# Optimization experiments

Hardware: AMD Instinct MI355X
Metric: run time of the kernel (lower is better)

## Reference

```python
import jax, jax.numpy as jnp
import numpy as np

B, C, L, D, P = 64, 64, 720, 512, 336
P2, H = P // 2, 512  # H = hidden width of the ProbG branch


def setup_inputs() -> dict:
    key = jax.random.key(0)
    ks = jax.random.split(key, 20)
    def w(k, i, o):
        return jax.random.normal(k, (i, o), jnp.float32) / np.sqrt(i)
    return {
        "x_bsd": jax.random.normal(ks[0], (B, L, C), jnp.float32),
        "z0": jax.random.normal(ks[1], (B, C, D), jnp.float32),
        "y0": jax.random.normal(ks[2], (B, C, P), jnp.float32),
        # ProbG hidden branch (HID_GIVEN_X_V0 -> SS_Z_GIVEN_X_V0)
        "W_h": w(ks[3], L, H),
        "W_ssz": w(ks[4], H, 2 * D),
        # x->z scale/shift flows (versions v2..v5)
        "W_xz_v2": w(ks[5], L, 2 * D),
        "W_xz_v3": w(ks[6], L, 2 * D),
        "W_xz_v4": w(ks[7], L, 2 * D),
        "W_xz_v5": w(ks[8], L, 2 * D),
        # z->x scale/shift flows (v0, v2, v3, v5)
        "W_zx_v0": w(ks[9], D, 2 * L),
        "W_zx_v2": w(ks[10], D, 2 * L),
        "W_zx_v3": w(ks[11], D, 2 * L),
        "W_zx_v5": w(ks[12], D, 2 * L),
        # z->y scale/shift flow (v4, used inside encoding)
        "W_zy_v4": w(ks[13], D, 2 * P),
        # decode heads: ROT_IN_Y_V1 and KOO_Y_GIVEN_Z_V0
        "W_rot": w(ks[14], D, P2),
        "W_koo": w(ks[15], D, 2 * P),
        # Koopman complex params for y-space (a + i b per channel/pair)
        "a_y": jnp.ones((C, P2), jnp.float32),
        "b_y": jnp.zeros((C, P2), jnp.float32) + 0.1,
    }


def _ss(params):
    """Split conditioner output into (positive scale, shift)."""
    s_raw, t = jnp.split(params, 2, axis=-1)
    return jnp.exp(jnp.tanh(s_raw)), t


def _affine(v, cond, W):
    """Scale/shift flow: v <- v * s(cond) + t(cond)."""
    s, t = _ss(jnp.einsum('bck,km->bcm', cond, W))
    return v * s + t


def _rot(u, theta, inv=False):
    """Rotate interleaved (re, im) pairs of u [B,C,P] by angles theta [B,C,P/2]."""
    re, im = u[..., 0::2], u[..., 1::2]
    th = -theta if inv else theta
    c, s = jnp.cos(th), jnp.sin(th)
    return jnp.stack([c * re - s * im, s * re + c * im], axis=-1).reshape(u.shape)


def _koop(u, a, b, inv=False):
    """Koopman unit-complex multiply on interleaved pairs; a,b [C,P/2]."""
    n = jnp.sqrt(a * a + b * b)
    ca, cb = a / n, b / n
    cb = -cb if inv else cb
    re, im = u[..., 0::2], u[..., 1::2]
    return jnp.stack([ca * re - cb * im, cb * re + ca * im], axis=-1).reshape(u.shape)


def reference(x_bsd, z0, y0, W_h, W_ssz, W_xz_v2, W_xz_v3, W_xz_v4, W_xz_v5,
              W_zx_v0, W_zx_v2, W_zx_v3, W_zx_v5, W_zy_v4, W_rot, W_koo, a_y, b_y):
    x = jnp.transpose(x_bsd, (0, 2, 1))  # [B,C,L]
    z = z0 * 0.1                          # [B,C,D]
    y = y0 * 0.1                          # [B,C,P]
    # ---- encoding phase ----
    h = jax.nn.gelu(jnp.einsum('bcl,lk->bck', x, W_h))  # X_to_Z_PROB hidden
    z = _affine(z, h, W_ssz)
    x = _affine(x, z, W_zx_v0)
    z = _affine(z, x, W_xz_v2); x = _affine(x, z, W_zx_v2)
    z = _affine(z, x, W_xz_v3); x = _affine(x, z, W_zx_v3)
    z = _affine(z, x, W_xz_v4); y = _affine(y, z, W_zy_v4)  # Z_to_Y_V4
    z = _affine(z, x, W_xz_v5); x = _affine(x, z, W_zx_v5)
    pre_y = y
    # ---- decode: rotate -> ky -> scale -> ky.inv -> rot.inv -> shift ----
    theta = jnp.pi * jnp.tanh(jnp.einsum('bcd,dp->bcp', z, W_rot))   # [B,C,P/2]
    scale, shift = _ss(jnp.einsum('bcd,dp->bcp', z, W_koo))          # [B,C,P]
    const = _koop(_rot(pre_y, theta), a_y, b_y)
    accu = const * scale
    accu = _rot(_koop(accu, a_y, b_y, inv=True), theta, inv=True) + shift
    return jnp.transpose(accu, (0, 2, 1))  # [B,P,C]
```

## Files before the change

kernel.cpp:

```cpp
#include <hip/hip_runtime.h>
#include <hip/hip_bf16.h>
#include <math.h>

#define BB  64
#define CC  64
#define LL  720
#define LLP 736
#define DD  512
#define PP  336
#define P2C 168
#define HH  512
#define MM  (BB*CC)

typedef _Float16 f16x8 __attribute__((ext_vector_type(8)));
typedef float    f32x4 __attribute__((ext_vector_type(4)));

#define GLDS16(g, l) __builtin_amdgcn_global_load_lds( \
    (const __attribute__((address_space(1))) void*)(g), \
    (__attribute__((address_space(3))) void*)(l), 16, 0, 0)

struct WDesc { const float* src; _Float16* dstHi; _Float16* dstLo;
               int K, N, Kpad, tbase, tilesN; };
struct WTab  { WDesc d[12]; };

__global__ __launch_bounds__(256) void k_convert(WTab tab) {
  __shared__ float tile[16][17];
  const int bid = blockIdx.x;
  int wi = 0;
#pragma unroll
  for (int i = 1; i < 12; ++i) if (bid >= tab.d[i].tbase) wi = i;
  const WDesc d = tab.d[wi];
  const int lt = bid - d.tbase;
  const int tk = lt / d.tilesN, tn = lt % d.tilesN;
  const int k0 = tk * 16, n0 = tn * 16;
  const int tx = threadIdx.x & 15, ty = threadIdx.x >> 4;
  float v = 0.f;
  if (n0 + tx < d.N) v = d.src[(size_t)(k0 + ty) * d.N + n0 + tx];
  tile[ty][tx] = v;
  __syncthreads();
  if (n0 + ty < d.N) {
    const float w = tile[tx][ty];
    const _Float16 h = (_Float16)w;
    const _Float16 l = (_Float16)(w - (float)h);
    const size_t base = (size_t)(n0 + ty) * d.Kpad;
    d.dstHi[base + k0 + tx] = h;
    d.dstLo[base + k0 + tx] = l;
    if (d.Kpad != d.K && k0 + 16 == d.K) {
      d.dstHi[base + d.K + tx] = (_Float16)0.f;
      d.dstLo[base + d.K + tx] = (_Float16)0.f;
    }
  }
}

__global__ __launch_bounds__(256) void k_xpose(const float* __restrict__ xbsd,
                                               _Float16* __restrict__ xhi,
                                               _Float16* __restrict__ xlo) {
  __shared__ float tile[16][17];
  const int b = blockIdx.z, l0 = blockIdx.x * 16, c0 = blockIdx.y * 16;
  const int tx = threadIdx.x, ty = threadIdx.y;
  tile[ty][tx] = xbsd[(size_t)b * LL * CC + (size_t)(l0 + ty) * CC + c0 + tx];
  __syncthreads();
  const float v = tile[tx][ty];
  const _Float16 h = (_Float16)v;
  const _Float16 l = (_Float16)(v - (float)h);
  const size_t m = (size_t)b * CC + c0 + ty;
  xhi[m * LLP + l0 + tx] = h;
  xlo[m * LLP + l0 + tx] = l;
  if (l0 == 704) {
    xhi[m * LLP + 720 + tx] = (_Float16)0.f;
    xlo[m * LLP + 720 + tx] = (_Float16)0.f;
  }
}

template<int EPI, bool DUAL, bool VIN16, bool OUT_T>
__global__ __launch_bounds__(256)
void k_gemm(const _Float16* Ahi, const _Float16* Alo, int lda,
            const _Float16* Whi, const _Float16* Wlo, int ldw,
            const float* Vin32, const _Float16* VinHi,
            const _Float16* VinLo, int ldv, float vscale,
            float* outT32,
            _Float16* outHi, _Float16* outLo, int ldo,
            int Kp, int Nv) {
  constexpr int NB   = DUAL ? 128 : 64;
  constexpr int BBUF = NB * 32;
  constexpr int SBUF = 2 * BBUF;
  constexpr int NCH  = 2 * (NB / 16);
  constexpr int NCHW = NCH / 4;
  __shared__ _Float16 smem[2 * SBUF];

  const int m0 = blockIdx.y * 64;
  const int n0 = blockIdx.x * 64;
  const int tid = threadIdx.x;
  const int w = tid >> 6, lane = tid & 63, q = lane >> 4, r = lane & 15;
  const int wr = (w & 1) * 32, wc = (w >> 1) * 32;
  const int lr = lane >> 2, ls = lane & 3;

  f32x4 accS[2][2] = {};
  f32x4 accT[2][2] = {};

  auto stage = [&](int kc, int bsel) {
    const int k0 = kc << 5;
    _Float16* sb = smem + bsel * SBUF;
#pragma unroll
    for (int cc = 0; cc < NCHW; ++cc) {
      const int chunk = w * NCHW + cc;
      const _Float16* gsrc;
      _Float16* ldst;
      if (chunk < NB / 16) {
        const int rb = chunk * 16;
        const int R = rb + lr;
        const int ss = ls ^ ((R >> 1) & 3);
        const int wrow = (R < 64) ? (n0 + R) : (Nv + n0 + (R - 64));
        gsrc = Whi + (size_t)wrow * ldw + k0 + ss * 8;
        ldst = sb + rb * 32;
      } else {
        const int rb = (chunk - NB / 16) * 16;
        const int R = rb + lr;
        const int ss = ls ^ ((R >> 1) & 3);
        const int wrow = (R < 64) ? (n0 + R) : (Nv + n0 + (R - 64));
        gsrc = Wlo + (size_t)wrow * ldw + k0 + ss * 8;
        ldst = sb + BBUF + rb * 32;
      }
      GLDS16(gsrc, ldst);
    }
  };

  const _Float16* aH0 = Ahi + (size_t)(m0 + wr + r)      * lda + q * 8;
  const _Float16* aH1 = Ahi + (size_t)(m0 + wr + 16 + r) * lda + q * 8;
  const _Float16* aL0 = Alo + (size_t)(m0 + wr + r)      * lda + q * 8;
  const _Float16* aL1 = Alo + (size_t)(m0 + wr + 16 + r) * lda + q * 8;

  const int nk = Kp >> 5;
  stage(0, 0);
  f16x8 c0h = *(const f16x8*)(aH0);
  f16x8 c1h = *(const f16x8*)(aH1);
  f16x8 c0l = *(const f16x8*)(aL0);
  f16x8 c1l = *(const f16x8*)(aL1);
  f16x8 p0h = c0h, p1h = c1h, p0l = c0l, p1l = c1l;
  int cur = 0;
  for (int kc = 0; kc < nk; ++kc) {
    __syncthreads();
    if (kc + 1 < nk) {
      stage(kc + 1, cur ^ 1);
      const int ko = (kc + 1) << 5;
      p0h = *(const f16x8*)(aH0 + ko);
      p1h = *(const f16x8*)(aH1 + ko);
      p0l = *(const f16x8*)(aL0 + ko);
      p1l = *(const f16x8*)(aL1 + ko);
    }
    const _Float16* sb = smem + cur * SBUF;

#pragma unroll
    for (int ct = 0; ct < 2; ++ct) {
      const int RB = wc + ct * 16 + r;
      const int tb = (q ^ ((RB >> 1) & 3)) * 8;
      const f16x8 bh = *(const f16x8*)(sb + RB * 32 + tb);
      const f16x8 bl = *(const f16x8*)(sb + BBUF + RB * 32 + tb);
      accS[0][ct] = __builtin_amdgcn_mfma_f32_16x16x32_f16(c0h, bh, accS[0][ct], 0, 0, 0);
      accS[0][ct] = __builtin_amdgcn_mfma_f32_16x16x32_f16(c0l, bh, accS[0][ct], 0, 0, 0);
      accS[0][ct] = __builtin_amdgcn_mfma_f32_16x16x32_f16(c0h, bl, accS[0][ct], 0, 0, 0);
      accS[1][ct] = __builtin_amdgcn_mfma_f32_16x16x32_f16(c1h, bh, accS[1][ct], 0, 0, 0);
      accS[1][ct] = __builtin_amdgcn_mfma_f32_16x16x32_f16(c1l, bh, accS[1][ct], 0, 0, 0);
      accS[1][ct] = __builtin_amdgcn_mfma_f32_16x16x32_f16(c1h, bl, accS[1][ct], 0, 0, 0);
      if (DUAL) {
        const int RT = 64 + RB;
        const int tt = (q ^ ((RT >> 1) & 3)) * 8;
        const f16x8 chh = *(const f16x8*)(sb + RT * 32 + tt);
        const f16x8 cll = *(const f16x8*)(sb + BBUF + RT * 32 + tt);
        accT[0][ct] = __builtin_amdgcn_mfma_f32_16x16x32_f16(c0h, chh, accT[0][ct], 0, 0, 0);
        accT[0][ct] = __builtin_amdgcn_mfma_f32_16x16x32_f16(c0l, chh, accT[0][ct], 0, 0, 0);
        accT[0][ct] = __builtin_amdgcn_mfma_f32_16x16x32_f16(c0h, cll, accT[0][ct], 0, 0, 0);
        accT[1][ct] = __builtin_amdgcn_mfma_f32_16x16x32_f16(c1h, chh, accT[1][ct], 0, 0, 0);
        accT[1][ct] = __builtin_amdgcn_mfma_f32_16x16x32_f16(c1l, chh, accT[1][ct], 0, 0, 0);
        accT[1][ct] = __builtin_amdgcn_mfma_f32_16x16x32_f16(c1h, cll, accT[1][ct], 0, 0, 0);
      }
    }
    c0h = p0h; c1h = p1h; c0l = p0l; c1l = p1l;
    cur ^= 1;
  }

#pragma unroll
  for (int rt = 0; rt < 2; ++rt) {
    const int mb = m0 + wr + rt * 16 + q * 4;
#pragma unroll
    for (int ct = 0; ct < 2; ++ct) {
      const int n = n0 + wc + ct * 16 + r;
      if (n >= Nv) continue;
      if (EPI == 2) {
        *(f32x4*)(outT32 + (size_t)n * MM + mb) = accS[rt][ct];
      } else if (EPI == 1) {
#pragma unroll
        for (int g = 0; g < 4; ++g) {
          const int m = mb + g;
          const float v = accS[rt][ct][g];
          const float o = 0.5f * v * (1.0f + tanhf(0.7978845608028654f * (v + 0.044715f * v * v * v)));
          const _Float16 h = (_Float16)o;
          outHi[(size_t)m * ldo + n] = h;
          outLo[(size_t)m * ldo + n] = (_Float16)(o - (float)h);
        }
      } else {
        f32x4 o;
#pragma unroll
        for (int g = 0; g < 4; ++g) {
          const int m = mb + g;
          float v;
          if (VIN16) {
            v = (float)VinHi[(size_t)m * ldv + n] + (float)VinLo[(size_t)m * ldv + n];
          } else {
            v = Vin32[(size_t)m * ldv + n];
          }
          const float s = expf(tanhf(accS[rt][ct][g]));
          o[g] = v * vscale * s + accT[rt][ct][g];
        }
        if (OUT_T) {
          *(f32x4*)(outT32 + (size_t)n * MM + mb) = o;
        } else {
#pragma unroll
          for (int g = 0; g < 4; ++g) {
            const int m = mb + g;
            const _Float16 h = (_Float16)o[g];
            outHi[(size_t)m * ldo + n] = h;
            outLo[(size_t)m * ldo + n] = (_Float16)(o[g] - (float)h);
          }
        }
      }
    }
  }
}

__global__ __launch_bounds__(256) void k_final(const float* __restrict__ Pt,
                                               const float* __restrict__ yT,
                                               const float* __restrict__ Ay,
                                               const float* __restrict__ By,
                                               float* __restrict__ out) {
  const int c = threadIdx.x;
  const int j = blockIdx.x * 4 + threadIdx.y;
  const int b = blockIdx.y;
  const int m = b * 64 + c;
  const float th = 3.14159265358979323846f * tanhf(Pt[(size_t)j * MM + m]);
  const float sc0 = expf(tanhf(Pt[(size_t)(168 + 2 * j) * MM + m]));
  const float sc1 = expf(tanhf(Pt[(size_t)(169 + 2 * j) * MM + m]));
  const float t0 = Pt[(size_t)(504 + 2 * j) * MM + m];
  const float t1 = Pt[(size_t)(505 + 2 * j) * MM + m];
  const float re = yT[(size_t)(2 * j) * MM + m];
  const float im = yT[(size_t)(2 * j + 1) * MM + m];
  const float a = Ay[c * P2C + j], bb = By[c * P2C + j];
  const float rn = rsqrtf(a * a + bb * bb);
  const float ca = a * rn, cb = bb * rn;
  float s1v, c1;
  sincosf(th, &s1v, &c1);
  const float r1 = c1 * re - s1v * im, i1 = s1v * re + c1 * im;
  const float r2 = ca * r1 - cb * i1,  i2 = cb * r1 + ca * i1;
  const float r3 = r2 * sc0,           i3 = i2 * sc1;
  const float r4 = ca * r3 + cb * i3,  i4 = ca * i3 - cb * r3;
  const float r5 = c1 * r4 + s1v * i4, i5 = c1 * i4 - s1v * r4;
  out[(size_t)b * PP * CC + (size_t)(2 * j) * CC + c]     = r5 + t0;
  out[(size_t)b * PP * CC + (size_t)(2 * j + 1) * CC + c] = i5 + t1;
}

extern "C" void kernel_launch(void* const* d_in, const int* in_sizes, int n_in,
                              void* d_out, int out_size, void* d_ws, size_t ws_size,
                              hipStream_t stream) {
  const float* x_bsd   = (const float*)d_in[0];
  const float* z0      = (const float*)d_in[1];
  const float* y0      = (const float*)d_in[2];
  const float* W_h     = (const float*)d_in[3];
  const float* W_ssz   = (const float*)d_in[4];
  const float* W_xz_v2 = (const float*)d_in[5];
  const float* W_xz_v3 = (const float*)d_in[6];
  const float* W_xz_v4 = (const float*)d_in[7];
  const float* W_xz_v5 = (const float*)d_in[8];
  const float* W_zx_v0 = (const float*)d_in[9];
  const float* W_zx_v2 = (const float*)d_in[10];
  const float* W_zx_v3 = (const float*)d_in[11];
  const float* W_zy_v4 = (const float*)d_in[13];
  const float* W_rot   = (const float*)d_in[14];
  const float* W_koo   = (const float*)d_in[15];
  const float* a_y     = (const float*)d_in[16];
  const float* b_y     = (const float*)d_in[17];
  float* out = (float*)d_out;

  char* p = (char*)d_ws;
  auto alloc = [&](size_t bytes) -> void* {
    void* r = (void*)p; p += (bytes + 255) & ~(size_t)255; return r;
  };
  float*    yT  = (float*)alloc((size_t)PP * MM * 4);
  float*    Pt  = (float*)alloc((size_t)(P2C * 5) * MM * 4);
  _Float16* xhi = (_Float16*)alloc((size_t)MM * LLP * 2);
  _Float16* xlo = (_Float16*)alloc((size_t)MM * LLP * 2);
  _Float16* zhi = (_Float16*)alloc((size_t)MM * DD * 2);
  _Float16* zlo = (_Float16*)alloc((size_t)MM * DD * 2);
  _Float16* hhi = (_Float16*)alloc((size_t)MM * HH * 2);
  _Float16* hlo = (_Float16*)alloc((size_t)MM * HH * 2);
  auto wpair = [&](size_t elems, _Float16** lo) -> _Float16* {
    _Float16* hi = (_Float16*)alloc(elems * 2);
    *lo = (_Float16*)alloc(elems * 2);
    return hi;
  };
  _Float16 *tWhL, *tWsszL, *tWxz2L, *tWxz3L, *tWxz4L, *tWxz5L;
  _Float16 *tWzx0L, *tWzx2L, *tWzx3L, *tWzyL, *tWcatL;
  _Float16* tWh   = wpair((size_t)HH * LLP, &tWhL);
  _Float16* tWssz = wpair((size_t)(2*DD) * DD, &tWsszL);
  _Float16* tWxz2 = wpair((size_t)(2*DD) * LLP, &tWxz2L);
  _Float16* tWxz3 = wpair((size_t)(2*DD) * LLP, &tWxz3L);
  _Float16* tWxz4 = wpair((size_t)(2*DD) * LLP, &tWxz4L);
  _Float16* tWxz5 = wpair((size_t)(2*DD) * LLP, &tWxz5L);
  _Float16* tWzx0 = wpair((size_t)1536 * DD, &tWzx0L);
  _Float16* tWzx2 = wpair((size_t)1536 * DD, &tWzx2L);
  _Float16* tWzx3 = wpair((size_t)1536 * DD, &tWzx3L);
  _Float16* tWzy  = wpair((size_t)768 * DD, &tWzyL);
  _Float16* tWcat = wpair((size_t)896 * DD, &tWcatL);

  WTab tab;
  int base = 0;
  auto put = [&](int i, const float* src, _Float16* dh, _Float16* dl,
                 int K, int N, int Kpad) {
    const int tN = (N + 15) / 16;
    tab.d[i] = WDesc{src, dh, dl, K, N, Kpad, base, tN};
    base += ((K + 15) / 16) * tN;
  };
  put(0,  W_h,     tWh,   tWhL,   LL, HH,   LLP);
  put(1,  W_ssz,   tWssz, tWsszL, DD, 2*DD, DD);
  put(2,  W_xz_v2, tWxz2, tWxz2L, LL, 2*DD, LLP);
  put(3,  W_xz_v3, tWxz3, tWxz3L, LL, 2*DD, LLP);
  put(4,  W_xz_v4, tWxz4, tWxz4L, LL, 2*DD, LLP);
  put(5,  W_xz_v5, tWxz5, tWxz5L, LL, 2*DD, LLP);
  put(6,  W_zx_v0, tWzx0, tWzx0L, DD, 2*LL, DD);
  put(7,  W_zx_v2, tWzx2, tWzx2L, DD, 2*LL, DD);
  put(8,  W_zx_v3, tWzx3, tWzx3L, DD, 2*LL, DD);
  put(9,  W_zy_v4, tWzy,  tWzyL,  DD, 2*PP, DD);
  put(10, W_rot,   tWcat, tWcatL, DD, P2C,  DD);
  put(11, W_koo,   tWcat + (size_t)P2C * DD, tWcatL + (size_t)P2C * DD, DD, 2*PP, DD);
  const int total_tiles = base;

  k_convert<<<dim3(total_tiles), dim3(256), 0, stream>>>(tab);
  k_xpose<<<dim3(45, 4, 64), dim3(16, 16), 0, stream>>>(x_bsd, xhi, xlo);

  const dim3 blk(256);
  k_gemm<1, false, false, false><<<dim3(8, 64), blk, 0, stream>>>(
      xhi, xlo, LLP, tWh, tWhL, LLP,
      nullptr, nullptr, nullptr, 0, 0.f, nullptr, hhi, hlo, HH, LLP, HH);
  k_gemm<0, true, false, false><<<dim3(8, 64), blk, 0, stream>>>(
      hhi, hlo, HH, tWssz, tWsszL, DD,
      z0, nullptr, nullptr, DD, 0.1f, nullptr, zhi, zlo, DD, DD, DD);
  k_gemm<0, true, true, false><<<dim3(12, 64), blk, 0, stream>>>(
      zhi, zlo, DD, tWzx0, tWzx0L, DD,
      nullptr, xhi, xlo, LLP, 1.f, nullptr, xhi, xlo, LLP, DD, LL);
  k_gemm<0, true, true, false><<<dim3(8, 64), blk, 0, stream>>>(
      xhi, xlo, LLP, tWxz2, tWxz2L, LLP,
      nullptr, zhi, zlo, DD, 1.f, nullptr, zhi, zlo, DD, LLP, DD);
  k_gemm<0, true, true, false><<<dim3(12, 64), blk, 0, stream>>>(
      zhi, zlo, DD, tWzx2, tWzx2L, DD,
      nullptr, xhi, xlo, LLP, 1.f, nullptr, xhi, xlo, LLP, DD, LL);
  k_gemm<0, true, true, false><<<dim3(8, 64), blk, 0, stream>>>(
      xhi, xlo, LLP, tWxz3, tWxz3L, LLP,
      nullptr, zhi, zlo, DD, 1.f, nullptr, zhi, zlo, DD, LLP, DD);
  k_gemm<0, true, true, false><<<dim3(12, 64), blk, 0, stream>>>(
      zhi, zlo, DD, tWzx3, tWzx3L, DD,
      nullptr, xhi, xlo, LLP, 1.f, nullptr, xhi, xlo, LLP, DD, LL);
  k_gemm<0, true, true, false><<<dim3(8, 64), blk, 0, stream>>>(
      xhi, xlo, LLP, tWxz4, tWxz4L, LLP,
      nullptr, zhi, zlo, DD, 1.f, nullptr, zhi, zlo, DD, LLP, DD);
  k_gemm<0, true, false, true><<<dim3(6, 64), blk, 0, stream>>>(
      zhi, zlo, DD, tWzy, tWzyL, DD,
      y0, nullptr, nullptr, PP, 0.1f, yT, nullptr, nullptr, 0, DD, PP);
  k_gemm<0, true, true, false><<<dim3(8, 64), blk, 0, stream>>>(
      xhi, xlo, LLP, tWxz5, tWxz5L, LLP,
      nullptr, zhi, zlo, DD, 1.f, nullptr, zhi, zlo, DD, LLP, DD);
  k_gemm<2, false, false, true><<<dim3(14, 64), blk, 0, stream>>>(
      zhi, zlo, DD, tWcat, tWcatL, DD,
      nullptr, nullptr, nullptr, 0, 0.f, Pt, nullptr, nullptr, 0, DD, P2C * 5);
  k_final<<<dim3(42, 64), dim3(64, 4), 0, stream>>>(Pt, yT, a_y, b_y, out);
}
```

Measured before the change: 514.9 us.

## Give each wave private B staging, swizzle block order, use fast transcendentals

After: 542.0 us. +5.3%, slower.

```diff
diff --git a/kernel.cpp b/kernel.cpp
--- a/kernel.cpp
+++ b/kernel.cpp
@@ -18,6 +18,13 @@
 #define GLDS16(g, l) __builtin_amdgcn_global_load_lds( \
     (const __attribute__((address_space(1))) void*)(g), \
     (__attribute__((address_space(3))) void*)(l), 16, 0, 0)
+
+__device__ __forceinline__ float ftanh(float x) {
+  const float ax = fabsf(x);
+  const float e  = __expf(2.f * ax);
+  const float t  = 1.f - 2.f / (e + 1.f);
+  return copysignf(t, x);
+}
 
 struct WDesc { const float* src; _Float16* dstHi; _Float16* dstLo;
                int K, N, Kpad, tbase, tilesN; };
@@ -81,47 +88,40 @@
             float* outT32,
             _Float16* outHi, _Float16* outLo, int ldo,
             int Kp, int Nv) {
-  constexpr int NB   = DUAL ? 128 : 64;
-  constexpr int BBUF = NB * 32;
-  constexpr int SBUF = 2 * BBUF;
-  constexpr int NCH  = 2 * (NB / 16);
-  constexpr int NCHW = NCH / 4;
-  __shared__ _Float16 smem[2 * SBUF];
-
-  const int m0 = blockIdx.y * 64;
-  const int n0 = blockIdx.x * 64;
+  constexpr int NBW  = DUAL ? 64 : 32;
+  constexpr int WBUF = NBW * 32;
+  constexpr int NCH  = 2 * (NBW / 16);
+  __shared__ _Float16 smem[4 * 2 * WBUF];
+
+  const int gx  = gridDim.x;
+  const int nwg = gx * gridDim.y;
+  const int id  = blockIdx.y * gx + blockIdx.x;
+  const int nid = (id & 7) * (nwg >> 3) + (id >> 3);
+  const int m0 = (nid / gx) * 64;
+  const int n0 = (nid % gx) * 64;
+
   const int tid = threadIdx.x;
   const int w = tid >> 6, lane = tid & 63, q = lane >> 4, r = lane & 15;
   const int wr = (w & 1) * 32, wc = (w >> 1) * 32;
   const int lr = lane >> 2, ls = lane & 3;
 
+  _Float16* wbase = smem + w * (2 * WBUF);
+
   f32x4 accS[2][2] = {};
   f32x4 accT[2][2] = {};
 
-  auto stage = [&](int kc, int bsel) {
+  auto stageB = [&](int kc) {
     const int k0 = kc << 5;
-    _Float16* sb = smem + bsel * SBUF;
-#pragma unroll
-    for (int cc = 0; cc < NCHW; ++cc) {
-      const int chunk = w * NCHW + cc;
-      const _Float16* gsrc;
-      _Float16* ldst;
-      if (chunk < NB / 16) {
-        const int rb = chunk * 16;
-        const int R = rb + lr;
-        const int ss = ls ^ ((R >> 1) & 3);
-        const int wrow = (R < 64) ? (n0 + R) : (Nv + n0 + (R - 64));
-        gsrc = Whi + (size_t)wrow * ldw + k0 + ss * 8;
-        ldst = sb + rb * 32;
-      } else {
-        const int rb = (chunk - NB / 16) * 16;
-        const int R = rb + lr;
-        const int ss = ls ^ ((R >> 1) & 3);
-        const int wrow = (R < 64) ? (n0 + R) : (Nv + n0 + (R - 64));
-        gsrc = Wlo + (size_t)wrow * ldw + k0 + ss * 8;
-        ldst = sb + BBUF + rb * 32;
-      }
-      GLDS16(gsrc, ldst);
+#pragma unroll
+    for (int cc = 0; cc < NCH; ++cc) {
+      const int pl   = (cc >= NCH / 2) ? 1 : 0;
+      const int rb   = (cc % (NCH / 2)) * 16;
+      const int lrow = rb + lr;
+      const int ss   = ls ^ ((lrow >> 1) & 3);
+      const int wrow = (lrow < 32) ? (n0 + wc + lrow)
+                                   : (Nv + n0 + wc + (lrow - 32));
+      const _Float16* g = (pl ? Wlo : Whi) + (size_t)wrow * ldw + k0 + ss * 8;
+      GLDS16(g, wbase + pl * WBUF + rb * 32);
     }
   };
 
@@ -131,52 +131,60 @@
   const _Float16* aL1 = Alo + (size_t)(m0 + wr + 16 + r) * lda + q * 8;
 
   const int nk = Kp >> 5;
-  stage(0, 0);
+  stageB(0);
   f16x8 c0h = *(const f16x8*)(aH0);
   f16x8 c1h = *(const f16x8*)(aH1);
   f16x8 c0l = *(const f16x8*)(aL0);
   f16x8 c1l = *(const f16x8*)(aL1);
   f16x8 p0h = c0h, p1h = c1h, p0l = c0l, p1l = c1l;
-  int cur = 0;
+
   for (int kc = 0; kc < nk; ++kc) {
-    __syncthreads();
+    asm volatile("s_waitcnt vmcnt(0)" ::: "memory");
+    __builtin_amdgcn_sched_barrier(0);
+
+    f16x8 bhS[2], blS[2], bhT[2], blT[2];
+#pragma unroll
+    for (int ct = 0; ct < 2; ++ct) {
+      const int rs = ct * 16 + r;
+      const int tb = (q ^ ((rs >> 1) & 3)) * 8;
+      bhS[ct] = *(const f16x8*)(wbase + rs * 32 + tb);
+      blS[ct] = *(const f16x8*)(wbase + WBUF + rs * 32 + tb);
+      if (DUAL) {
+        const int rt2 = 32 + ct * 16 + r;
+        const int tt = (q ^ ((rt2 >> 1) & 3)) * 8;
+        bhT[ct] = *(const f16x8*)(wbase + rt2 * 32 + tt);
+        blT[ct] = *(const f16x8*)(wbase + WBUF + rt2 * 32 + tt);
+      }
+    }
+    asm volatile("s_waitcnt lgkmcnt(0)" ::: "memory");
+    __builtin_amdgcn_sched_barrier(0);
     if (kc + 1 < nk) {
-      stage(kc + 1, cur ^ 1);
+      stageB(kc + 1);
       const int ko = (kc + 1) << 5;
       p0h = *(const f16x8*)(aH0 + ko);
       p1h = *(const f16x8*)(aH1 + ko);
       p0l = *(const f16x8*)(aL0 + ko);
       p1l = *(const f16x8*)(aL1 + ko);
     }
-    const _Float16* sb = smem + cur * SBUF;
 
 #pragma unroll
     for (int ct = 0; ct < 2; ++ct) {
-      const int RB = wc + ct * 16 + r;
-      const int tb = (q ^ ((RB >> 1) & 3)) * 8;
-      const f16x8 bh = *(const f16x8*)(sb + RB * 32 + tb);
-      const f16x8 bl = *(const f16x8*)(sb + BBUF + RB * 32 + tb);
-      accS[0][ct] = __builtin_amdgcn_mfma_f32_16x16x32_f16(c0h, bh, accS[0][ct], 0, 0, 0);
-      accS[0][ct] = __builtin_amdgcn_mfma_f32_16x16x32_f16(c0l, bh, accS[0][ct], 0, 0, 0);
-      accS[0][ct] = __builtin_amdgcn_mfma_f32_16x16x32_f16(c0h, bl, accS[0][ct], 0, 0, 0);
-      accS[1][ct] = __builtin_amdgcn_mfma_f32_16x16x32_f16(c1h, bh, accS[1][ct], 0, 0, 0);
-      accS[1][ct] = __builtin_amdgcn_mfma_f32_16x16x32_f16(c1l, bh, accS[1][ct], 0, 0, 0);
-      accS[1][ct] = __builtin_amdgcn_mfma_f32_16x16x32_f16(c1h, bl, accS[1][ct], 0, 0, 0);
+      accS[0][ct] = __builtin_amdgcn_mfma_f32_16x16x32_f16(c0h, bhS[ct], accS[0][ct], 0, 0, 0);
+      accS[0][ct] = __builtin_amdgcn_mfma_f32_16x16x32_f16(c0l, bhS[ct], accS[0][ct], 0, 0, 0);
+      accS[0][ct] = __builtin_amdgcn_mfma_f32_16x16x32_f16(c0h, blS[ct], accS[0][ct], 0, 0, 0);
+      accS[1][ct] = __builtin_amdgcn_mfma_f32_16x16x32_f16(c1h, bhS[ct], accS[1][ct], 0, 0, 0);
+      accS[1][ct] = __builtin_amdgcn_mfma_f32_16x16x32_f16(c1l, bhS[ct], accS[1][ct], 0, 0, 0);
+      accS[1][ct] = __builtin_amdgcn_mfma_f32_16x16x32_f16(c1h, blS[ct], accS[1][ct], 0, 0, 0);
       if (DUAL) {
-        const int RT = 64 + RB;
-        const int tt = (q ^ ((RT >> 1) & 3)) * 8;
-        const f16x8 chh = *(const f16x8*)(sb + RT * 32 + tt);
-        const f16x8 cll = *(const f16x8*)(sb + BBUF + RT * 32 + tt);
-        accT[0][ct] = __builtin_amdgcn_mfma_f32_16x16x32_f16(c0h, chh, accT[0][ct], 0, 0, 0);
-        accT[0][ct] = __builtin_amdgcn_mfma_f32_16x16x32_f16(c0l, chh, accT[0][ct], 0, 0, 0);
-        accT[0][ct] = __builtin_amdgcn_mfma_f32_16x16x32_f16(c0h, cll, accT[0][ct], 0, 0, 0);
-        accT[1][ct] = __builtin_amdgcn_mfma_f32_16x16x32_f16(c1h, chh, accT[1][ct], 0, 0, 0);
-        accT[1][ct] = __builtin_amdgcn_mfma_f32_16x16x32_f16(c1l, chh, accT[1][ct], 0, 0, 0);
-        accT[1][ct] = __builtin_amdgcn_mfma_f32_16x16x32_f16(c1h, cll, accT[1][ct], 0, 0, 0);
+        accT[0][ct] = __builtin_amdgcn_mfma_f32_16x16x32_f16(c0h, bhT[ct], accT[0][ct], 0, 0, 0);
+        accT[0][ct] = __builtin_amdgcn_mfma_f32_16x16x32_f16(c0l, bhT[ct], accT[0][ct], 0, 0, 0);
+        accT[0][ct] = __builtin_amdgcn_mfma_f32_16x16x32_f16(c0h, blT[ct], accT[0][ct], 0, 0, 0);
+        accT[1][ct] = __builtin_amdgcn_mfma_f32_16x16x32_f16(c1h, bhT[ct], accT[1][ct], 0, 0, 0);
+        accT[1][ct] = __builtin_amdgcn_mfma_f32_16x16x32_f16(c1l, bhT[ct], accT[1][ct], 0, 0, 0);
+        accT[1][ct] = __builtin_amdgcn_mfma_f32_16x16x32_f16(c1h, blT[ct], accT[1][ct], 0, 0, 0);
       }
     }
     c0h = p0h; c1h = p1h; c0l = p0l; c1l = p1l;
-    cur ^= 1;
   }
 
 #pragma unroll
@@ -193,7 +201,7 @@
         for (int g = 0; g < 4; ++g) {
           const int m = mb + g;
           const float v = accS[rt][ct][g];
-          const float o = 0.5f * v * (1.0f + tanhf(0.7978845608028654f * (v + 0.044715f * v * v * v)));
+          const float o = 0.5f * v * (1.0f + ftanh(0.7978845608028654f * (v + 0.044715f * v * v * v)));
           const _Float16 h = (_Float16)o;
           outHi[(size_t)m * ldo + n] = h;
           outLo[(size_t)m * ldo + n] = (_Float16)(o - (float)h);
@@ -209,7 +217,7 @@
           } else {
             v = Vin32[(size_t)m * ldv + n];
           }
-          const float s = expf(tanhf(accS[rt][ct][g]));
+          const float s = __expf(ftanh(accS[rt][ct][g]));
           o[g] = v * vscale * s + accT[rt][ct][g];
         }
         if (OUT_T) {
@@ -237,9 +245,9 @@
   const int j = blockIdx.x * 4 + threadIdx.y;
   const int b = blockIdx.y;
   const int m = b * 64 + c;
-  const float th = 3.14159265358979323846f * tanhf(Pt[(size_t)j * MM + m]);
-  const float sc0 = expf(tanhf(Pt[(size_t)(168 + 2 * j) * MM + m]));
-  const float sc1 = expf(tanhf(Pt[(size_t)(169 + 2 * j) * MM + m]));
+  const float th = 3.14159265358979323846f * ftanh(Pt[(size_t)j * MM + m]);
+  const float sc0 = __expf(ftanh(Pt[(size_t)(168 + 2 * j) * MM + m]));
+  const float sc1 = __expf(ftanh(Pt[(size_t)(169 + 2 * j) * MM + m]));
   const float t0 = Pt[(size_t)(504 + 2 * j) * MM + m];
   const float t1 = Pt[(size_t)(505 + 2 * j) * MM + m];
   const float re = yT[(size_t)(2 * j) * MM + m];
@@ -248,7 +256,7 @@
   const float rn = rsqrtf(a * a + bb * bb);
   const float ca = a * rn, cb = bb * rn;
   float s1v, c1;
-  sincosf(th, &s1v, &c1);
+  __sincosf(th, &s1v, &c1);
   const float r1 = c1 * re - s1v * im, i1 = s1v * re + c1 * im;
   const float r2 = ca * r1 - cb * i1,  i2 = cb * r1 + ca * i1;
   const float r3 = r2 * sc0,           i3 = i2 * sc1;
```
